# Kernel tuning notes

Hardware: AMD Instinct MI355X
Metric: run time of the kernel (lower is better)

Reference implementation:

```python
import jax, jax.numpy as jnp
import numpy as np

D_MODEL = 1024
HEAD_DIM = D_MODEL // 16  # num_heads=16, used only for the softmax scale
EPS = 1e-5


def _layernorm(x, g, b):
    mu = jnp.mean(x, axis=-1, keepdims=True)
    var = jnp.var(x, axis=-1, keepdims=True)
    return (x - mu) * jax.lax.rsqrt(var + EPS) * g + b


def setup_inputs() -> dict:
    key = jax.random.key(0)
    ks = jax.random.split(key, 16)
    d, dff = D_MODEL, 4 * D_MODEL
    s = 1.0 / np.sqrt(d)
    inp = {
        "x": jax.random.normal(ks[0], (4, 2048, d), dtype=jnp.float32),
        "wq": jax.random.normal(ks[1], (d, d), dtype=jnp.float32) * s,
        "bq": jnp.zeros((d,), jnp.float32),
        "wk": jax.random.normal(ks[2], (d, d), dtype=jnp.float32) * s,
        "bk": jnp.zeros((d,), jnp.float32),
        "wv": jax.random.normal(ks[3], (d, d), dtype=jnp.float32) * s,
        "bv": jnp.zeros((d,), jnp.float32),
        "wo": jax.random.normal(ks[4], (d, d), dtype=jnp.float32) * s,
        "bo": jnp.zeros((d,), jnp.float32),
        "w1": jax.random.normal(ks[5], (d, dff), dtype=jnp.float32) * s,
        "b1": jnp.zeros((dff,), jnp.float32),
        "w2": jax.random.normal(ks[6], (dff, d), dtype=jnp.float32) * (1.0 / np.sqrt(dff)),
        "b2": jnp.zeros((d,), jnp.float32),
        "g1": jnp.ones((d,), jnp.float32),
        "be1": jnp.zeros((d,), jnp.float32),
        "g2": jnp.ones((d,), jnp.float32),
        "be2": jnp.zeros((d,), jnp.float32),
    }
    return inp


def reference(x, wq, bq, wk, bk, wv, bv, wo, bo, w1, b1, w2, b2, g1, be1, g2, be2):
    # --- attention sub-block (NOTE: no head split in original module) ---
    residual = x
    h = _layernorm(x, g1, be1)
    q = h @ wq + bq
    k = h @ wk + bk
    v = h @ wv + bv
    scale = 1.0 / np.sqrt(HEAD_DIM)
    scores = jnp.einsum("bsd,btd->bst", q, k) * scale  # [B,S,S]
    attn = jax.nn.softmax(scores, axis=-1)
    ctx = jnp.einsum("bst,btd->bsd", attn, v)
    x = ctx @ wo + bo + residual
    # --- MLP sub-block ---
    residual = x
    h = _layernorm(x, g2, be2)
    h = jax.nn.gelu(h @ w1 + b1, approximate=False)
    return h @ w2 + b2 + residual
```

## Files before the change

kernel.cpp:

```cpp
#include <hip/hip_runtime.h>
#include <hip/hip_bf16.h>

typedef __hip_bfloat16 bf16;
typedef __attribute__((ext_vector_type(8))) short short8;
typedef __attribute__((ext_vector_type(4))) float floatx4;
typedef __attribute__((address_space(3))) char c3;

template <int V> struct ic { static constexpr int value = V; };

__device__ __forceinline__ unsigned short f2bf(float x) {
  unsigned u = __builtin_bit_cast(unsigned, x);
  unsigned r = (u + 0x7fffu + ((u >> 16) & 1u)) >> 16;
  return (unsigned short)r;
}

#define GLL(g, l) __builtin_amdgcn_global_load_lds(                                  \
    (const __attribute__((address_space(1))) void*)(g),                              \
    (__attribute__((address_space(3))) void*)(l), 16, 0, 0)

template <int N> __device__ __forceinline__ void vmwait() {
  asm volatile("s_waitcnt vmcnt(%0)" ::"i"(N) : "memory");
}
template <int N> __device__ __forceinline__ void lgkwait() {
  asm volatile("s_waitcnt lgkmcnt(%0)" ::"i"(N) : "memory");
  __builtin_amdgcn_sched_barrier(0);
}
template <int OFF> __device__ __forceinline__ short8 dsr(unsigned a) {
  short8 r;
  asm volatile("ds_read_b128 %0, %1 offset:%2" : "=v"(r) : "v"(a), "i"(OFF));
  return r;
}
#define MFMA_(d, a, b) d = __builtin_amdgcn_mfma_f32_16x16x32_bf16(a, b, d, 0, 0, 0)

__global__ __launch_bounds__(256) void wtrans_kernel(const float* __restrict__ in,
                                                     bf16* __restrict__ out,
                                                     int K, int N) {
  __shared__ float tile[32][33];
  int tx = threadIdx.x, ty = threadIdx.y;
  int n0 = blockIdx.x * 32, k0 = blockIdx.y * 32;
#pragma unroll
  for (int i = 0; i < 32; i += 8)
    tile[ty + i][tx] = in[(size_t)(k0 + ty + i) * N + (n0 + tx)];
  __syncthreads();
#pragma unroll
  for (int i = 0; i < 32; i += 8)
    out[(size_t)(n0 + ty + i) * K + (k0 + tx)] = __float2bfloat16(tile[tx][ty + i]);
}

__global__ __launch_bounds__(256) void ln_kernel(const float* __restrict__ x,
                                                 const float* __restrict__ g,
                                                 const float* __restrict__ b,
                                                 bf16* __restrict__ out) {
  const int D = 1024;
  size_t row = blockIdx.x;
  int t = threadIdx.x;
  float4 v = ((const float4*)(x + row * D))[t];
  float s  = v.x + v.y + v.z + v.w;
  float ss = v.x * v.x + v.y * v.y + v.z * v.z + v.w * v.w;
#pragma unroll
  for (int off = 32; off > 0; off >>= 1) {
    s  += __shfl_xor(s, off);
    ss += __shfl_xor(ss, off);
  }
  __shared__ float rs[4], rss[4];
  int wv = t >> 6;
  if ((t & 63) == 0) { rs[wv] = s; rss[wv] = ss; }
  __syncthreads();
  s  = rs[0] + rs[1] + rs[2] + rs[3];
  ss = rss[0] + rss[1] + rss[2] + rss[3];
  float mu  = s * (1.f / D);
  float inv = rsqrtf(ss * (1.f / D) - mu * mu + 1e-5f);
  float4 gv = ((const float4*)g)[t];
  float4 bv = ((const float4*)b)[t];
  ushort4 o;
  o.x = f2bf((v.x - mu) * inv * gv.x + bv.x);
  o.y = f2bf((v.y - mu) * inv * gv.y + bv.y);
  o.z = f2bf((v.z - mu) * inv * gv.z + bv.z);
  o.w = f2bf((v.w - mu) * inv * gv.w + bv.w);
  ((ushort4*)(out + row * D))[t] = o;
}

__global__ __launch_bounds__(256) void softmax_kernel(float* sc) {
  const int S = 2048;
  float* p = sc + (size_t)blockIdx.x * S;
  int t = threadIdx.x;
  float4 v0 = ((const float4*)p)[2 * t];
  float4 v1 = ((const float4*)p)[2 * t + 1];
  float f[8] = {v0.x, v0.y, v0.z, v0.w, v1.x, v1.y, v1.z, v1.w};
  float m = f[0];
#pragma unroll
  for (int j = 1; j < 8; ++j) m = fmaxf(m, f[j]);
#pragma unroll
  for (int off = 32; off > 0; off >>= 1) m = fmaxf(m, __shfl_xor(m, off));
  __shared__ float r1[4], r2[4];
  int wv = t >> 6;
  if ((t & 63) == 0) r1[wv] = m;
  __syncthreads();
  m = fmaxf(fmaxf(r1[0], r1[1]), fmaxf(r1[2], r1[3]));
  float s = 0.f;
#pragma unroll
  for (int j = 0; j < 8; ++j) { f[j] = __expf(f[j] - m); s += f[j]; }
#pragma unroll
  for (int off = 32; off > 0; off >>= 1) s += __shfl_xor(s, off);
  if ((t & 63) == 0) r2[wv] = s;
  __syncthreads();
  s = r2[0] + r2[1] + r2[2] + r2[3];
  float inv = 1.f / s;
  unsigned u0 = f2bf(f[0] * inv), u1 = f2bf(f[1] * inv);
  unsigned u2 = f2bf(f[2] * inv), u3 = f2bf(f[3] * inv);
  unsigned u4 = f2bf(f[4] * inv), u5 = f2bf(f[5] * inv);
  unsigned u6 = f2bf(f[6] * inv), u7 = f2bf(f[7] * inv);
  uint4 o;
  o.x = u0 | (u1 << 16);
  o.y = u2 | (u3 << 16);
  o.z = u4 | (u5 << 16);
  o.w = u6 | (u7 << 16);
  ((uint4*)p)[t] = o;
}

template <bool OUT_BF16, bool HAS_BIAS, bool HAS_RES, bool GELU, bool VTR>
__global__ __launch_bounds__(512, 2) void gemm9w(
    const bf16* __restrict__ A, int lda, size_t sA,
    const bf16* __restrict__ BT, int ldb, size_t sB,
    void* Cv, size_t sC,
    const float* __restrict__ bias, const float* res, bf16* vtr,
    int N, int K, float alpha, int gx, int gy) {
  __shared__ __align__(16) char ldsb[131072];
  const unsigned lds0 = (unsigned)(uintptr_t)(c3*)ldsb;

  const int tid = threadIdx.x;
  const int lane = tid & 63;
  const int wave = tid >> 6;
  const int wm = wave >> 2, wn = wave & 3;
  const int lr = lane & 15, lq = lane >> 4;

  int id = blockIdx.x;
  const int nwg = gridDim.x;
  if ((nwg & 7) == 0) id = (id & 7) * (nwg >> 3) + (id >> 3);
  const int bx = id % gx;
  const int rem = id / gx;
  const int by = rem % gy;
  const int bz = rem / gy;
  const int m0 = by * 256, n0 = bx * 256;

  const int sidx = tid >> 3;
  const int schunk = ((tid & 7) ^ (sidx & 7)) * 8;
  const bf16* gA = A + sA * bz + (size_t)(m0 + sidx) * lda + schunk;
  const int rowB = ((sidx >> 5) << 6) + (sidx & 31);
  const bf16* gB = BT + sB * bz + (size_t)(n0 + rowB) * ldb + schunk;

  const int nk = K >> 6;

  auto stA = [&](int tt, int h) {
    if (tt < nk) {
      const bf16* s = gA + (size_t)(h * 64) * lda + (size_t)tt * 64;
      char* d = ldsb + (((tt & 1) * 2 + h) << 14) + tid * 16;
      GLL(s, d);
      GLL(s + (size_t)128 * lda, d + 8192);
    }
  };
  auto stB = [&](int tt, int g) {
    if (tt < nk) {
      const bf16* s = gB + (size_t)(g * 32) * ldb + (size_t)tt * 64;
      char* d = ldsb + 65536 + (((tt & 1) * 2 + g) << 14) + tid * 16;
      GLL(s, d);
      GLL(s + (size_t)128 * ldb, d + 8192);
    }
  };

  const unsigned aoff = (wm * 64 + lr) * 128 + ((lq ^ (lr & 7)) << 4);
  const unsigned boff = (wn * 32 + lr) * 128 + ((lq ^ (lr & 7)) << 4);

  floatx4 acc[2][2][4][2] = {};

  stA(0, 0); stB(0, 0); stB(0, 1); stA(0, 1);
  stA(1, 0); stB(1, 0); stB(1, 1);
  vmwait<6>();
  __builtin_amdgcn_s_barrier();

  auto body = [&](int kt, auto modeC) {
    constexpr int MODE = decltype(modeC)::value;
    const unsigned p = (unsigned)(kt & 1);
    const unsigned Aa = lds0 + ((p * 2 + 0) << 14);
    const unsigned Ab = lds0 + ((p * 2 + 1) << 14);
    const unsigned Bg = lds0 + 65536 + ((p * 2 + 0) << 14);
    const unsigned Bd = lds0 + 65536 + ((p * 2 + 1) << 14);
    short8 a0[4], a1[4], g0[2], g1[2], d0[2], d1[2];

    {
      const unsigned aA = Aa + aoff, aX = aA ^ 64;
      a0[0] = dsr<0>(aA); a0[1] = dsr<2048>(aA); a0[2] = dsr<4096>(aA); a0[3] = dsr<6144>(aA);
      a1[0] = dsr<0>(aX); a1[1] = dsr<2048>(aX); a1[2] = dsr<4096>(aX); a1[3] = dsr<6144>(aX);
      const unsigned bA = Bg + boff, bX = bA ^ 64;
      g0[0] = dsr<0>(bA); g0[1] = dsr<2048>(bA);
      g1[0] = dsr<0>(bX); g1[1] = dsr<2048>(bX);
    }
    stA(kt + 1, 1);
    __builtin_amdgcn_s_barrier();
    lgkwait<0>();
    __builtin_amdgcn_s_setprio(1);
#pragma unroll
    for (int mi = 0; mi < 4; ++mi)
#pragma unroll
      for (int nl = 0; nl < 2; ++nl) MFMA_(acc[0][0][mi][nl], a0[mi], g0[nl]);
#pragma unroll
    for (int mi = 0; mi < 4; ++mi)
#pragma unroll
      for (int nl = 0; nl < 2; ++nl) MFMA_(acc[0][0][mi][nl], a1[mi], g1[nl]);
    __builtin_amdgcn_s_setprio(0);
    __builtin_amdgcn_s_barrier();

    {
      const unsigned bA = Bd + boff, bX = bA ^ 64;
      d0[0] = dsr<0>(bA); d0[1] = dsr<2048>(bA);
      d1[0] = dsr<0>(bX); d1[1] = dsr<2048>(bX);
    }
    stA(kt + 2, 0);
    __builtin_amdgcn_s_barrier();
    lgkwait<0>();
    __builtin_amdgcn_s_setprio(1);
#pragma unroll
    for (int mi = 0; mi < 4; ++mi)
#pragma unroll
      for (int nl = 0; nl < 2; ++nl) MFMA_(acc[0][1][mi][nl], a0[mi], d0[nl]);
#pragma unroll
    for (int mi = 0; mi < 4; ++mi)
#pragma unroll
      for (int nl = 0; nl < 2; ++nl) MFMA_(acc[0][1][mi][nl], a1[mi], d1[nl]);
    __builtin_amdgcn_s_setprio(0);
    __builtin_amdgcn_s_barrier();

    {
      const unsigned aA = Ab + aoff, aX = aA ^ 64;
      a0[0] = dsr<0>(aA); a0[1] = dsr<2048>(aA); a0[2] = dsr<4096>(aA); a0[3] = dsr<6144>(aA);
      a1[0] = dsr<0>(aX); a1[1] = dsr<2048>(aX); a1[2] = dsr<4096>(aX); a1[3] = dsr<6144>(aX);
    }
    stB(kt + 2, 0);
    __builtin_amdgcn_s_barrier();
    lgkwait<0>();
    __builtin_amdgcn_s_setprio(1);
#pragma unroll
    for (int mi = 0; mi < 4; ++mi)
#pragma unroll
      for (int nl = 0; nl < 2; ++nl) MFMA_(acc[1][1][mi][nl], a0[mi], d0[nl]);
#pragma unroll
    for (int mi = 0; mi < 4; ++mi)
#pragma unroll
      for (int nl = 0; nl < 2; ++nl) MFMA_(acc[1][1][mi][nl], a1[mi], d1[nl]);
    __builtin_amdgcn_s_setprio(0);
    __builtin_amdgcn_s_barrier();

    stB(kt + 2, 1);
    __builtin_amdgcn_s_barrier();
    __builtin_amdgcn_s_setprio(1);
#pragma unroll
    for (int mi = 0; mi < 4; ++mi)
#pragma unroll
      for (int nl = 0; nl < 2; ++nl) MFMA_(acc[1][0][mi][nl], a0[mi], g0[nl]);
#pragma unroll
    for (int mi = 0; mi < 4; ++mi)
#pragma unroll
      for (int nl = 0; nl < 2; ++nl) MFMA_(acc[1][0][mi][nl], a1[mi], g1[nl]);
    __builtin_amdgcn_s_setprio(0);
    if constexpr (MODE == 0) vmwait<6>();
    else if constexpr (MODE == 1) vmwait<0>();
    __builtin_amdgcn_s_barrier();
  };

  for (int kt = 0; kt + 2 < nk; ++kt) body(kt, ic<0>{});
  body(nk - 2, ic<1>{});
  body(nk - 1, ic<2>{});

  float* Cf = (float*)Cv;
  bf16* Cb = (bf16*)Cv;
  const size_t cb = sC * bz;
#pragma unroll
  for (int mh = 0; mh < 2; ++mh)
#pragma unroll
    for (int ng = 0; ng < 2; ++ng)
#pragma unroll
      for (int mi = 0; mi < 4; ++mi) {
        const int row = m0 + wm * 128 + (mh * 4 + mi) * 16 + lq * 4;
#pragma unroll
        for (int nl = 0; nl < 2; ++nl) {
          const int col = n0 + wn * 64 + (ng * 2 + nl) * 16 + lr;
          const float bb = HAS_BIAS ? bias[col] : 0.f;
#pragma unroll
          for (int r = 0; r < 4; ++r) {
            float val = acc[mh][ng][mi][nl][r] * alpha + bb;
            if (GELU) val = 0.5f * val * (1.f + erff(val * 0.70710678118654752f));
            if (HAS_RES) val += res[(size_t)(row + r) * N + col];
            const size_t idx = cb + (size_t)(row + r) * N + col;
            if (OUT_BF16) Cb[idx] = __float2bfloat16(val);
            else Cf[idx] = val;
            if (VTR) {
              if (col >= 2048) {
                const int rr = row + r;
                vtr[(((size_t)(rr >> 11) << 10) + (col - 2048)) * 2048 + (rr & 2047)] =
                    __float2bfloat16(val);
              }
            }
          }
        }
      }
}

template <bool OUT_BF16, bool HAS_BIAS, bool HAS_RES, bool GELU, bool VTR>
__global__ __launch_bounds__(512, 2) void gemm9n(
    const bf16* __restrict__ A, int lda, size_t sA,
    const bf16* __restrict__ BT, int ldb, size_t sB,
    void* Cv, size_t sC,
    const float* __restrict__ bias, const float* res, bf16* vtr,
    int N, int K, float alpha, int gx, int gy) {
  __shared__ __align__(16) char ldsb[98304];
  const unsigned lds0 = (unsigned)(uintptr_t)(c3*)ldsb;

  const int tid = threadIdx.x;
  const int lane = tid & 63;
  const int wave = tid >> 6;
  const int wm = wave >> 2, wn = wave & 3;
  const int lr = lane & 15, lq = lane >> 4;

  int id = blockIdx.x;
  const int nwg = gridDim.x;
  if ((nwg & 7) == 0) id = (id & 7) * (nwg >> 3) + (id >> 3);
  const int bx = id % gx;
  const int rem = id / gx;
  const int by = rem % gy;
  const int bz = rem / gy;
  const int m0 = by * 256, n0 = bx * 128;

  const int sidx = tid >> 3;
  const int schunk = ((tid & 7) ^ (sidx & 7)) * 8;
  const bf16* gA = A + sA * bz + (size_t)(m0 + sidx) * lda + schunk;
  const bf16* gB = BT + sB * bz + (size_t)(n0 + sidx) * ldb + schunk;

  const int nk = K >> 6;

  auto stA = [&](int tt, int h) {
    if (tt < nk) {
      const bf16* s = gA + (size_t)(h * 64) * lda + (size_t)tt * 64;
      char* d = ldsb + (((tt & 1) * 2 + h) << 14) + tid * 16;
      GLL(s, d);
      GLL(s + (size_t)128 * lda, d + 8192);
    }
  };
  auto stBn = [&](int tt) {
    if (tt < nk) {
      const bf16* s = gB + (size_t)tt * 64;
      char* d = ldsb + 65536 + ((tt & 1) << 14) + tid * 16;
      GLL(s, d);
      GLL(s + (size_t)64 * ldb, d + 8192);
    }
  };

  const unsigned aoff = (wm * 64 + lr) * 128 + ((lq ^ (lr & 7)) << 4);
  const unsigned boff = (wn * 32 + lr) * 128 + ((lq ^ (lr & 7)) << 4);

  floatx4 acc[2][4][2] = {};

  stA(0, 0); stBn(0); stA(0, 1);
  stA(1, 0); stBn(1);
  vmwait<4>();
  __builtin_amdgcn_s_barrier();

  auto body = [&](int kt, auto modeC) {
    constexpr int MODE = decltype(modeC)::value;
    const unsigned p = (unsigned)(kt & 1);
    const unsigned Aa = lds0 + ((p * 2 + 0) << 14);
    const unsigned Ab = lds0 + ((p * 2 + 1) << 14);
    const unsigned Bb = lds0 + 65536 + (p << 14);
    short8 a0[4], a1[4], b0[2], b1[2];

    {
      const unsigned aA = Aa + aoff, aX = aA ^ 64;
      a0[0] = dsr<0>(aA); a0[1] = dsr<2048>(aA); a0[2] = dsr<4096>(aA); a0[3] = dsr<6144>(aA);
      a1[0] = dsr<0>(aX); a1[1] = dsr<2048>(aX); a1[2] = dsr<4096>(aX); a1[3] = dsr<6144>(aX);
      const unsigned bA = Bb + boff, bX = bA ^ 64;
      b0[0] = dsr<0>(bA); b0[1] = dsr<2048>(bA);
      b1[0] = dsr<0>(bX); b1[1] = dsr<2048>(bX);
    }
    stA(kt + 1, 1);
    __builtin_amdgcn_s_barrier();
    lgkwait<0>();
    __builtin_amdgcn_s_setprio(1);
#pragma unroll
    for (int mi = 0; mi < 4; ++mi)
#pragma unroll
      for (int nl = 0; nl < 2; ++nl) MFMA_(acc[0][mi][nl], a0[mi], b0[nl]);
#pragma unroll
    for (int mi = 0; mi < 4; ++mi)
#pragma unroll
      for (int nl = 0; nl < 2; ++nl) MFMA_(acc[0][mi][nl], a1[mi], b1[nl]);
    __builtin_amdgcn_s_setprio(0);
    __builtin_amdgcn_s_barrier();

    {
      const unsigned aA = Ab + aoff, aX = aA ^ 64;
      a0[0] = dsr<0>(aA); a0[1] = dsr<2048>(aA); a0[2] = dsr<4096>(aA); a0[3] = dsr<6144>(aA);
      a1[0] = dsr<0>(aX); a1[1] = dsr<2048>(aX); a1[2] = dsr<4096>(aX); a1[3] = dsr<6144>(aX);
    }
    stA(kt + 2, 0); stBn(kt + 2);
    __builtin_amdgcn_s_barrier();
    lgkwait<0>();
    __builtin_amdgcn_s_setprio(1);
#pragma unroll
    for (int mi = 0; mi < 4; ++mi)
#pragma unroll
      for (int nl = 0; nl < 2; ++nl) MFMA_(acc[1][mi][nl], a0[mi], b0[nl]);
#pragma unroll
    for (int mi = 0; mi < 4; ++mi)
#pragma unroll
      for (int nl = 0; nl < 2; ++nl) MFMA_(acc[1][mi][nl], a1[mi], b1[nl]);
    __builtin_amdgcn_s_setprio(0);
    if constexpr (MODE == 0) vmwait<4>();
    else if constexpr (MODE == 1) vmwait<0>();
    __builtin_amdgcn_s_barrier();
  };

  for (int kt = 0; kt + 2 < nk; ++kt) body(kt, ic<0>{});
  body(nk - 2, ic<1>{});
  body(nk - 1, ic<2>{});

  float* Cf = (float*)Cv;
  bf16* Cb = (bf16*)Cv;
  const size_t cb = sC * bz;
#pragma unroll
  for (int mh = 0; mh < 2; ++mh)
#pragma unroll
    for (int mi = 0; mi < 4; ++mi) {
      const int row = m0 + wm * 128 + (mh * 4 + mi) * 16 + lq * 4;
#pragma unroll
      for (int nl = 0; nl < 2; ++nl) {
        const int col = n0 + wn * 32 + nl * 16 + lr;
        const float bb = HAS_BIAS ? bias[col] : 0.f;
#pragma unroll
        for (int r = 0; r < 4; ++r) {
          float val = acc[mh][mi][nl][r] * alpha + bb;
          if (GELU) val = 0.5f * val * (1.f + erff(val * 0.70710678118654752f));
          if (HAS_RES) val += res[(size_t)(row + r) * N + col];
          const size_t idx = cb + (size_t)(row + r) * N + col;
          if (OUT_BF16) Cb[idx] = __float2bfloat16(val);
          else Cf[idx] = val;
          if (VTR) {
            if (col >= 2048) {
              const int rr = row + r;
              vtr[(((size_t)(rr >> 11) << 10) + (col - 2048)) * 2048 + (rr & 2047)] =
                  __float2bfloat16(val);
            }
          }
        }
      }
    }
}

extern "C" void kernel_launch(void* const* d_in, const int* in_sizes, int n_in,
                              void* d_out, int out_size, void* d_ws, size_t ws_size,
                              hipStream_t stream) {
  const int B = 4, S = 2048, D = 1024, DFF = 4096;
  const int M = B * S;
  const float* x   = (const float*)d_in[0];
  const float* wq  = (const float*)d_in[1];
  const float* bq  = (const float*)d_in[2];
  const float* wk  = (const float*)d_in[3];
  const float* bk  = (const float*)d_in[4];
  const float* wv  = (const float*)d_in[5];
  const float* bv  = (const float*)d_in[6];
  const float* wo  = (const float*)d_in[7];
  const float* bo  = (const float*)d_in[8];
  const float* w1  = (const float*)d_in[9];
  const float* b1  = (const float*)d_in[10];
  const float* w2  = (const float*)d_in[11];
  const float* b2  = (const float*)d_in[12];
  const float* g1  = (const float*)d_in[13];
  const float* be1 = (const float*)d_in[14];
  const float* g2  = (const float*)d_in[15];
  const float* be2 = (const float*)d_in[16];
  float* out = (float*)d_out;

  char* wsb = (char*)d_ws;
  const size_t MB1 = 1ull << 20;
  bf16* wqkvT = (bf16*)(wsb + 0 * MB1);
  bf16* woT   = (bf16*)(wsb + 6 * MB1);
  bf16* w1T   = (bf16*)(wsb + 8 * MB1);
  bf16* w2T   = (bf16*)(wsb + 16 * MB1);
  float* bqkv = (float*)(wsb + 24 * MB1);
  bf16* h     = (bf16*)(wsb + 25 * MB1);
  bf16* qkv   = (bf16*)(wsb + 41 * MB1);
  bf16* hidden = (bf16*)(wsb + 41 * MB1);
  bf16* vTall = (bf16*)(wsb + 89 * MB1);
  float* sc   = (float*)(wsb + 105 * MB1);

  int chunk = 1;
  if (ws_size > 105 * MB1) {
    size_t c = (ws_size - 105 * MB1) / (16 * MB1);
    chunk = (int)(c > 4 ? 4 : (c < 1 ? 1 : c));
  }

  dim3 tb(32, 8);
  wtrans_kernel<<<dim3(32, 32), tb, 0, stream>>>(wq, wqkvT, D, D);
  wtrans_kernel<<<dim3(32, 32), tb, 0, stream>>>(wk, wqkvT + (size_t)1024 * 1024, D, D);
  wtrans_kernel<<<dim3(32, 32), tb, 0, stream>>>(wv, wqkvT + (size_t)2048 * 1024, D, D);
  wtrans_kernel<<<dim3(32, 32), tb, 0, stream>>>(wo, woT, D, D);
  wtrans_kernel<<<dim3(128, 32), tb, 0, stream>>>(w1, w1T, D, DFF);
  wtrans_kernel<<<dim3(32, 128), tb, 0, stream>>>(w2, w2T, DFF, D);
  hipMemcpyAsync(bqkv, bq, 4096, hipMemcpyDeviceToDevice, stream);
  hipMemcpyAsync(bqkv + 1024, bk, 4096, hipMemcpyDeviceToDevice, stream);
  hipMemcpyAsync(bqkv + 2048, bv, 4096, hipMemcpyDeviceToDevice, stream);

  ln_kernel<<<M, 256, 0, stream>>>(x, g1, be1, h);

  gemm9w<true, true, false, false, true><<<12 * 32, 512, 0, stream>>>(
      h, D, 0, wqkvT, D, 0, qkv, 0, bqkv, nullptr, vTall, 3072, D, 1.f, 12, 32);

  for (int b0 = 0; b0 < B; b0 += chunk) {
    int c = (B - b0 < chunk) ? (B - b0) : chunk;
    gemm9w<false, false, false, false, false><<<64 * c, 512, 0, stream>>>(
        qkv + (size_t)b0 * S * 3072, 3072, (size_t)S * 3072,
        qkv + (size_t)b0 * S * 3072 + 1024, 3072, (size_t)S * 3072,
        sc, (size_t)S * S, nullptr, nullptr, nullptr, S, D, 0.125f, 8, 8);
    softmax_kernel<<<c * S, 256, 0, stream>>>(sc);
    gemm9n<true, false, false, false, false><<<64 * c, 512, 0, stream>>>(
        (const bf16*)sc, 2 * S, (size_t)S * 2 * S,
        vTall + (size_t)b0 * D * S, S, (size_t)D * S,
        h + (size_t)b0 * S * D, (size_t)S * D, nullptr, nullptr, nullptr, D, S, 1.f, 8, 8);
  }

  gemm9n<false, true, true, false, false><<<8 * 32, 512, 0, stream>>>(
      h, D, 0, woT, D, 0, out, 0, bo, x, nullptr, D, D, 1.f, 8, 32);

  ln_kernel<<<M, 256, 0, stream>>>(out, g2, be2, h);

  gemm9w<true, true, false, true, false><<<16 * 32, 512, 0, stream>>>(
      h, D, 0, w1T, D, 0, hidden, 0, b1, nullptr, nullptr, DFF, D, 1.f, 16, 32);

  gemm9n<false, true, true, false, false><<<8 * 32, 512, 0, stream>>>(
      hidden, DFF, 0, w2T, DFF, 0, out, 0, b2, out, nullptr, D, DFF, 1.f, 8, 32);
}
```

Before: 469.6 us.

## Switch GEMM kernels to 32x32x16 MFMA with K-split LDS staging

Both GEMM kernels move from 16x16x32 bf16 MFMA to 32x32x16 bf16 MFMA. The LDS tiles are restaged so that each K-tile is split into two 32-wide K halves with a 4-chunk XOR swizzle, and each body iteration now has two phases instead of four, with fewer barriers. The goal is fewer MFMA instructions and fewer LDS reads per FLOP, plus less synchronisation. The risks are LDS bank conflicts from the new swizzle and a changed wait-count pipeline, and the epilogue now writes strided 32x32 output fragments.

```diff
diff --git a/kernel.cpp b/kernel.cpp
--- a/kernel.cpp
+++ b/kernel.cpp
@@ -3,7 +3,7 @@
 
 typedef __hip_bfloat16 bf16;
 typedef __attribute__((ext_vector_type(8))) short short8;
-typedef __attribute__((ext_vector_type(4))) float floatx4;
+typedef __attribute__((ext_vector_type(16))) float floatx16;
 typedef __attribute__((address_space(3))) char c3;
 
 template <int V> struct ic { static constexpr int value = V; };
@@ -30,7 +30,7 @@
   asm volatile("ds_read_b128 %0, %1 offset:%2" : "=v"(r) : "v"(a), "i"(OFF));
   return r;
 }
-#define MFMA_(d, a, b) d = __builtin_amdgcn_mfma_f32_16x16x32_bf16(a, b, d, 0, 0, 0)
+#define MFMA32(d, a, b) d = __builtin_amdgcn_mfma_f32_32x32x16_bf16(a, b, d, 0, 0, 0)
 
 __global__ __launch_bounds__(256) void wtrans_kernel(const float* __restrict__ in,
                                                      bf16* __restrict__ out,
@@ -119,7 +119,7 @@
 }
 
 template <bool OUT_BF16, bool HAS_BIAS, bool HAS_RES, bool GELU, bool VTR>
-__global__ __launch_bounds__(512, 2) void gemm9w(
+__global__ __launch_bounds__(512, 2) void gemmA(
     const bf16* __restrict__ A, int lda, size_t sA,
     const bf16* __restrict__ BT, int ldb, size_t sB,
     void* Cv, size_t sC,
@@ -127,12 +127,13 @@
     int N, int K, float alpha, int gx, int gy) {
   __shared__ __align__(16) char ldsb[131072];
   const unsigned lds0 = (unsigned)(uintptr_t)(c3*)ldsb;
+  const unsigned ldsB0 = lds0 + 65536;
 
   const int tid = threadIdx.x;
   const int lane = tid & 63;
   const int wave = tid >> 6;
   const int wm = wave >> 2, wn = wave & 3;
-  const int lr = lane & 15, lq = lane >> 4;
+  const int l5 = lane >> 5, l31 = lane & 31;
 
   int id = blockIdx.x;
   const int nwg = gridDim.x;
@@ -143,128 +144,96 @@
   const int bz = rem / gy;
   const int m0 = by * 256, n0 = bx * 256;
 
-  const int sidx = tid >> 3;
-  const int schunk = ((tid & 7) ^ (sidx & 7)) * 8;
-  const bf16* gA = A + sA * bz + (size_t)(m0 + sidx) * lda + schunk;
-  const int rowB = ((sidx >> 5) << 6) + (sidx & 31);
-  const bf16* gB = BT + sB * bz + (size_t)(n0 + rowB) * ldb + schunk;
-
+  const int sr = tid >> 2;
+  const int scc = ((tid & 3) ^ (sr & 3)) * 8;
+  const bf16* gA = A + sA * bz + (size_t)(m0 + sr) * lda + scc;
+  const bf16* gB = BT + sB * bz + (size_t)(n0 + sr) * ldb + scc;
   const int nk = K >> 6;
 
-  auto stA = [&](int tt, int h) {
+  auto stA = [&](int tt, int kh) {
     if (tt < nk) {
-      const bf16* s = gA + (size_t)(h * 64) * lda + (size_t)tt * 64;
-      char* d = ldsb + (((tt & 1) * 2 + h) << 14) + tid * 16;
+      const bf16* s = gA + (size_t)tt * 64 + kh * 32;
+      char* d = ldsb + (((tt & 1) * 2 + kh) << 14) + tid * 16;
       GLL(s, d);
       GLL(s + (size_t)128 * lda, d + 8192);
     }
   };
-  auto stB = [&](int tt, int g) {
+  auto stB = [&](int tt, int kh) {
     if (tt < nk) {
-      const bf16* s = gB + (size_t)(g * 32) * ldb + (size_t)tt * 64;
-      char* d = ldsb + 65536 + (((tt & 1) * 2 + g) << 14) + tid * 16;
+      const bf16* s = gB + (size_t)tt * 64 + kh * 32;
+      char* d = ldsb + 65536 + (((tt & 1) * 2 + kh) << 14) + tid * 16;
       GLL(s, d);
       GLL(s + (size_t)128 * ldb, d + 8192);
     }
   };
 
-  const unsigned aoff = (wm * 64 + lr) * 128 + ((lq ^ (lr & 7)) << 4);
-  const unsigned boff = (wn * 32 + lr) * 128 + ((lq ^ (lr & 7)) << 4);
-
-  floatx4 acc[2][2][4][2] = {};
-
-  stA(0, 0); stB(0, 0); stB(0, 1); stA(0, 1);
-  stA(1, 0); stB(1, 0); stB(1, 1);
-  vmwait<6>();
+  const unsigned uswz = (unsigned)((l5 ^ (lane & 3)) << 4);
+  const unsigned aRow = (unsigned)((wm * 128 + l31) * 64) + uswz;
+  const unsigned bRow = (unsigned)((wn * 64 + l31) * 64) + uswz;
+
+  floatx16 acc[4][2] = {};
+
+  stA(0, 0); stB(0, 0);
+  stA(0, 1); stB(0, 1);
+  stA(1, 0); stB(1, 0);
+  vmwait<8>();
   __builtin_amdgcn_s_barrier();
 
   auto body = [&](int kt, auto modeC) {
     constexpr int MODE = decltype(modeC)::value;
     const unsigned p = (unsigned)(kt & 1);
-    const unsigned Aa = lds0 + ((p * 2 + 0) << 14);
-    const unsigned Ab = lds0 + ((p * 2 + 1) << 14);
-    const unsigned Bg = lds0 + 65536 + ((p * 2 + 0) << 14);
-    const unsigned Bd = lds0 + 65536 + ((p * 2 + 1) << 14);
-    short8 a0[4], a1[4], g0[2], g1[2], d0[2], d1[2];
+    const unsigned Ak0 = lds0 + ((p * 2 + 0) << 14);
+    const unsigned Ak1 = lds0 + ((p * 2 + 1) << 14);
+    const unsigned Bk0 = ldsB0 + ((p * 2 + 0) << 14);
+    const unsigned Bk1 = ldsB0 + ((p * 2 + 1) << 14);
+    short8 a0[4], a1[4], b0[2], b1[2];
 
     {
-      const unsigned aA = Aa + aoff, aX = aA ^ 64;
+      const unsigned aA = Ak0 + aRow, aX = aA ^ 32;
       a0[0] = dsr<0>(aA); a0[1] = dsr<2048>(aA); a0[2] = dsr<4096>(aA); a0[3] = dsr<6144>(aA);
       a1[0] = dsr<0>(aX); a1[1] = dsr<2048>(aX); a1[2] = dsr<4096>(aX); a1[3] = dsr<6144>(aX);
-      const unsigned bA = Bg + boff, bX = bA ^ 64;
-      g0[0] = dsr<0>(bA); g0[1] = dsr<2048>(bA);
-      g1[0] = dsr<0>(bX); g1[1] = dsr<2048>(bX);
-    }
-    stA(kt + 1, 1);
-    __builtin_amdgcn_s_barrier();
+      const unsigned bA = Bk0 + bRow, bX = bA ^ 32;
+      b0[0] = dsr<0>(bA); b0[1] = dsr<2048>(bA);
+      b1[0] = dsr<0>(bX); b1[1] = dsr<2048>(bX);
+    }
+    stA(kt + 1, 1); stB(kt + 1, 1);
     lgkwait<0>();
     __builtin_amdgcn_s_setprio(1);
 #pragma unroll
-    for (int mi = 0; mi < 4; ++mi)
-#pragma unroll
-      for (int nl = 0; nl < 2; ++nl) MFMA_(acc[0][0][mi][nl], a0[mi], g0[nl]);
-#pragma unroll
-    for (int mi = 0; mi < 4; ++mi)
-#pragma unroll
-      for (int nl = 0; nl < 2; ++nl) MFMA_(acc[0][0][mi][nl], a1[mi], g1[nl]);
+    for (int mf = 0; mf < 4; ++mf)
+#pragma unroll
+      for (int nf = 0; nf < 2; ++nf) MFMA32(acc[mf][nf], a0[mf], b0[nf]);
+#pragma unroll
+    for (int mf = 0; mf < 4; ++mf)
+#pragma unroll
+      for (int nf = 0; nf < 2; ++nf) MFMA32(acc[mf][nf], a1[mf], b1[nf]);
     __builtin_amdgcn_s_setprio(0);
+    if constexpr (MODE < 2) vmwait<8>();
+    else vmwait<0>();
     __builtin_amdgcn_s_barrier();
 
     {
-      const unsigned bA = Bd + boff, bX = bA ^ 64;
-      d0[0] = dsr<0>(bA); d0[1] = dsr<2048>(bA);
-      d1[0] = dsr<0>(bX); d1[1] = dsr<2048>(bX);
-    }
-    stA(kt + 2, 0);
-    __builtin_amdgcn_s_barrier();
+      const unsigned aA = Ak1 + aRow, aX = aA ^ 32;
+      a0[0] = dsr<0>(aA); a0[1] = dsr<2048>(aA); a0[2] = dsr<4096>(aA); a0[3] = dsr<6144>(aA);
+      a1[0] = dsr<0>(aX); a1[1] = dsr<2048>(aX); a1[2] = dsr<4096>(aX); a1[3] = dsr<6144>(aX);
+      const unsigned bA = Bk1 + bRow, bX = bA ^ 32;
+      b0[0] = dsr<0>(bA); b0[1] = dsr<2048>(bA);
+      b1[0] = dsr<0>(bX); b1[1] = dsr<2048>(bX);
+    }
+    stA(kt + 2, 0); stB(kt + 2, 0);
     lgkwait<0>();
     __builtin_amdgcn_s_setprio(1);
 #pragma unroll
-    for (int mi = 0; mi < 4; ++mi)
-#pragma unroll
-      for (int nl = 0; nl < 2; ++nl) MFMA_(acc[0][1][mi][nl], a0[mi], d0[nl]);
-#pragma unroll
-    for (int mi = 0; mi < 4; ++mi)
-#pragma unroll
-      for (int nl = 0; nl < 2; ++nl) MFMA_(acc[0][1][mi][nl], a1[mi], d1[nl]);
+    for (int mf = 0; mf < 4; ++mf)
+#pragma unroll
+      for (int nf = 0; nf < 2; ++nf) MFMA32(acc[mf][nf], a0[mf], b0[nf]);
+#pragma unroll
+    for (int mf = 0; mf < 4; ++mf)
+#pragma unroll
+      for (int nf = 0; nf < 2; ++nf) MFMA32(acc[mf][nf], a1[mf], b1[nf]);
     __builtin_amdgcn_s_setprio(0);
-    __builtin_amdgcn_s_barrier();
-
-    {
-      const unsigned aA = Ab + aoff, aX = aA ^ 64;
-      a0[0] = dsr<0>(aA); a0[1] = dsr<2048>(aA); a0[2] = dsr<4096>(aA); a0[3] = dsr<6144>(aA);
-      a1[0] = dsr<0>(aX); a1[1] = dsr<2048>(aX); a1[2] = dsr<4096>(aX); a1[3] = dsr<6144>(aX);
-    }
-    stB(kt + 2, 0);
-    __builtin_amdgcn_s_barrier();
-    lgkwait<0>();
-    __builtin_amdgcn_s_setprio(1);
-#pragma unroll
-    for (int mi = 0; mi < 4; ++mi)
-#pragma unroll
-      for (int nl = 0; nl < 2; ++nl) MFMA_(acc[1][1][mi][nl], a0[mi], d0[nl]);
-#pragma unroll
-    for (int mi = 0; mi < 4; ++mi)
-#pragma unroll
-      for (int nl = 0; nl < 2; ++nl) MFMA_(acc[1][1][mi][nl], a1[mi], d1[nl]);
-    __builtin_amdgcn_s_setprio(0);
-    __builtin_amdgcn_s_barrier();
-
-    stB(kt + 2, 1);
-    __builtin_amdgcn_s_barrier();
-    __builtin_amdgcn_s_setprio(1);
-#pragma unroll
-    for (int mi = 0; mi < 4; ++mi)
-#pragma unroll
-      for (int nl = 0; nl < 2; ++nl) MFMA_(acc[1][0][mi][nl], a0[mi], g0[nl]);
-#pragma unroll
-    for (int mi = 0; mi < 4; ++mi)
-#pragma unroll
-      for (int nl = 0; nl < 2; ++nl) MFMA_(acc[1][0][mi][nl], a1[mi], g1[nl]);
-    __builtin_amdgcn_s_setprio(0);
-    if constexpr (MODE == 0) vmwait<6>();
-    else if constexpr (MODE == 1) vmwait<0>();
-    __builtin_amdgcn_s_barrier();
+    if constexpr (MODE == 0) { vmwait<8>(); __builtin_amdgcn_s_barrier(); }
+    else if constexpr (MODE == 1) { vmwait<4>(); __builtin_amdgcn_s_barrier(); }
   };
 
   for (int kt = 0; kt + 2 < nk; ++kt) body(kt, ic<0>{});
@@ -274,52 +243,49 @@
   float* Cf = (float*)Cv;
   bf16* Cb = (bf16*)Cv;
   const size_t cb = sC * bz;
-#pragma unroll
-  for (int mh = 0; mh < 2; ++mh)
-#pragma unroll
-    for (int ng = 0; ng < 2; ++ng)
-#pragma unroll
-      for (int mi = 0; mi < 4; ++mi) {
-        const int row = m0 + wm * 128 + (mh * 4 + mi) * 16 + lq * 4;
-#pragma unroll
-        for (int nl = 0; nl < 2; ++nl) {
-          const int col = n0 + wn * 64 + (ng * 2 + nl) * 16 + lr;
-          const float bb = HAS_BIAS ? bias[col] : 0.f;
-#pragma unroll
-          for (int r = 0; r < 4; ++r) {
-            float val = acc[mh][ng][mi][nl][r] * alpha + bb;
-            if (GELU) val = 0.5f * val * (1.f + erff(val * 0.70710678118654752f));
-            if (HAS_RES) val += res[(size_t)(row + r) * N + col];
-            const size_t idx = cb + (size_t)(row + r) * N + col;
-            if (OUT_BF16) Cb[idx] = __float2bfloat16(val);
-            else Cf[idx] = val;
-            if (VTR) {
-              if (col >= 2048) {
-                const int rr = row + r;
-                vtr[(((size_t)(rr >> 11) << 10) + (col - 2048)) * 2048 + (rr & 2047)] =
-                    __float2bfloat16(val);
-              }
-            }
+  const int colb = n0 + wn * 64 + l31;
+  const int rowb = m0 + wm * 128 + (l5 << 2);
+#pragma unroll
+  for (int mf = 0; mf < 4; ++mf)
+#pragma unroll
+    for (int nf = 0; nf < 2; ++nf) {
+      const int col = colb + nf * 32;
+      const float bb = HAS_BIAS ? bias[col] : 0.f;
+#pragma unroll
+      for (int r = 0; r < 16; ++r) {
+        const int row = rowb + mf * 32 + (r & 3) + ((r >> 2) << 3);
+        float val = acc[mf][nf][r] * alpha + bb;
+        if (GELU) val = 0.5f * val * (1.f + erff(val * 0.70710678118654752f));
+        if (HAS_RES) val += res[(size_t)row * N + col];
+        const size_t idx = cb + (size_t)row * N + col;
+        if (OUT_BF16) Cb[idx] = __float2bfloat16(val);
+        else Cf[idx] = val;
+        if (VTR) {
+          if (col >= 2048) {
+            vtr[(((size_t)(row >> 11) << 10) + (col - 2048)) * 2048 + (row & 2047)] =
+                __float2bfloat16(val);
           }
         }
       }
-}
-
-template <bool OUT_BF16, bool HAS_BIAS, bool HAS_RES, bool GELU, bool VTR>
-__global__ __launch_bounds__(512, 2) void gemm9n(
+    }
+}
+
+template <bool OUT_BF16, bool HAS_BIAS, bool HAS_RES, bool GELU>
+__global__ __launch_bounds__(512, 2) void gemmB(
     const bf16* __restrict__ A, int lda, size_t sA,
     const bf16* __restrict__ BT, int ldb, size_t sB,
     void* Cv, size_t sC,
-    const float* __restrict__ bias, const float* res, bf16* vtr,
+    const float* __restrict__ bias, const float* res,
     int N, int K, float alpha, int gx, int gy) {
   __shared__ __align__(16) char ldsb[98304];
   const unsigned lds0 = (unsigned)(uintptr_t)(c3*)ldsb;
+  const unsigned ldsB0 = lds0 + 65536;
 
   const int tid = threadIdx.x;
   const int lane = tid & 63;
   const int wave = tid >> 6;
   const int wm = wave >> 2, wn = wave & 3;
-  const int lr = lane & 15, lq = lane >> 4;
+  const int l5 = lane >> 5, l31 = lane & 31;
 
   int id = blockIdx.x;
   const int nwg = gridDim.x;
@@ -330,92 +296,85 @@
   const int bz = rem / gy;
   const int m0 = by * 256, n0 = bx * 128;
 
-  const int sidx = tid >> 3;
-  const int schunk = ((tid & 7) ^ (sidx & 7)) * 8;
-  const bf16* gA = A + sA * bz + (size_t)(m0 + sidx) * lda + schunk;
-  const bf16* gB = BT + sB * bz + (size_t)(n0 + sidx) * ldb + schunk;
-
+  const int sr = tid >> 2;
+  const int scc = ((tid & 3) ^ (sr & 3)) * 8;
+  const bf16* gA = A + sA * bz + (size_t)(m0 + sr) * lda + scc;
+  const bf16* gB = BT + sB * bz + (size_t)(n0 + sr) * ldb + scc;
   const int nk = K >> 6;
 
-  auto stA = [&](int tt, int h) {
+  auto stA = [&](int tt, int kh) {
     if (tt < nk) {
-      const bf16* s = gA + (size_t)(h * 64) * lda + (size_t)tt * 64;
-      char* d = ldsb + (((tt & 1) * 2 + h) << 14) + tid * 16;
+      const bf16* s = gA + (size_t)tt * 64 + kh * 32;
+      char* d = ldsb + (((tt & 1) * 2 + kh) << 14) + tid * 16;
       GLL(s, d);
       GLL(s + (size_t)128 * lda, d + 8192);
     }
   };
-  auto stBn = [&](int tt) {
+  auto stB = [&](int tt, int kh) {
     if (tt < nk) {
-      const bf16* s = gB + (size_t)tt * 64;
-      char* d = ldsb + 65536 + ((tt & 1) << 14) + tid * 16;
+      const bf16* s = gB + (size_t)tt * 64 + kh * 32;
+      char* d = ldsb + 65536 + (((tt & 1) * 2 + kh) << 13) + tid * 16;
       GLL(s, d);
-      GLL(s + (size_t)64 * ldb, d + 8192);
-    }
-  };
-
-  const unsigned aoff = (wm * 64 + lr) * 128 + ((lq ^ (lr & 7)) << 4);
-  const unsigned boff = (wn * 32 + lr) * 128 + ((lq ^ (lr & 7)) << 4);
-
-  floatx4 acc[2][4][2] = {};
-
-  stA(0, 0); stBn(0); stA(0, 1);
-  stA(1, 0); stBn(1);
-  vmwait<4>();
+    }
+  };
+
+  const unsigned uswz = (unsigned)((l5 ^ (lane & 3)) << 4);
+  const unsigned aRow = (unsigned)((wm * 128 + l31) * 64) + uswz;
+  const unsigned bRow = (unsigned)((wn * 32 + l31) * 64) + uswz;
+
+  floatx16 acc[4] = {};
+
+  stA(0, 0); stB(0, 0);
+  stA(0, 1); stB(0, 1);
+  stA(1, 0); stB(1, 0);
+  vmwait<6>();
   __builtin_amdgcn_s_barrier();
 
   auto body = [&](int kt, auto modeC) {
     constexpr int MODE = decltype(modeC)::value;
     const unsigned p = (unsigned)(kt & 1);
-    const unsigned Aa = lds0 + ((p * 2 + 0) << 14);
-    const unsigned Ab = lds0 + ((p * 2 + 1) << 14);
-    const unsigned Bb = lds0 + 65536 + (p << 14);
-    short8 a0[4], a1[4], b0[2], b1[2];
+    const unsigned Ak0 = lds0 + ((p * 2 + 0) << 14);
+    const unsigned Ak1 = lds0 + ((p * 2 + 1) << 14);
+    const unsigned Bk0 = ldsB0 + ((p * 2 + 0) << 13);
+    const unsigned Bk1 = ldsB0 + ((p * 2 + 1) << 13);
+    short8 a0[4], a1[4], b0, b1;
 
     {
-      const unsigned aA = Aa + aoff, aX = aA ^ 64;
+      const unsigned aA = Ak0 + aRow, aX = aA ^ 32;
       a0[0] = dsr<0>(aA); a0[1] = dsr<2048>(aA); a0[2] = dsr<4096>(aA); a0[3] = dsr<6144>(aA);
       a1[0] = dsr<0>(aX); a1[1] = dsr<2048>(aX); a1[2] = dsr<4096>(aX); a1[3] = dsr<6144>(aX);
-      const unsigned bA = Bb + boff, bX = bA ^ 64;
-      b0[0] = dsr<0>(bA); b0[1] = dsr<2048>(bA);
-      b1[0] = dsr<0>(bX); b1[1] = dsr<2048>(bX);
-    }
-    stA(kt + 1, 1);
-    __builtin_amdgcn_s_barrier();
+      const unsigned bA = Bk0 + bRow;
+      b0 = dsr<0>(bA); b1 = dsr<0>(bA ^ 32);
+    }
+    stA(kt + 1, 1); stB(kt + 1, 1);
     lgkwait<0>();
     __builtin_amdgcn_s_setprio(1);
 #pragma unroll
-    for (int mi = 0; mi < 4; ++mi)
-#pragma unroll
-      for (int nl = 0; nl < 2; ++nl) MFMA_(acc[0][mi][nl], a0[mi], b0[nl]);
-#pragma unroll
-    for (int mi = 0; mi < 4; ++mi)
-#pragma unroll
-      for (int nl = 0; nl < 2; ++nl) MFMA_(acc[0][mi][nl], a1[mi], b1[nl]);
+    for (int mf = 0; mf < 4; ++mf) MFMA32(acc[mf], a0[mf], b0);
+#pragma unroll
+    for (int mf = 0; mf < 4; ++mf) MFMA32(acc[mf], a1[mf], b1);
     __builtin_amdgcn_s_setprio(0);
+    if constexpr (MODE < 2) vmwait<6>();
+    else vmwait<0>();
     __builtin_amdgcn_s_barrier();
 
     {
-      const unsigned aA = Ab + aoff, aX = aA ^ 64;
+      const unsigned aA = Ak1 + aRow, aX = aA ^ 32;
       a0[0] = dsr<0>(aA); a0[1] = dsr<2048>(aA); a0[2] = dsr<4096>(aA); a0[3] = dsr<6144>(aA);
       a1[0] = dsr<0>(aX); a1[1] = dsr<2048>(aX); a1[2] = dsr<4096>(aX); a1[3] = dsr<6144>(aX);
-    }
-    stA(kt + 2, 0); stBn(kt + 2);
-    __builtin_amdgcn_s_barrier();
+      const unsigned bA = Bk1 + bRow;
+      b0 = dsr<0>(bA); b1 = dsr<0>(bA ^ 32);
+    }
+    stA(kt + 2, 0); stB(kt + 2, 0);
     lgkwait<0>();
     __builtin_amdgcn_s_setprio(1);
 #pragma unroll
-    for (int mi = 0; mi < 4; ++mi)
-#pragma unroll
-      for (int nl = 0; nl < 2; ++nl) MFMA_(acc[1][mi][nl], a0[mi], b0[nl]);
-#pragma unroll
-    for (int mi = 0; mi < 4; ++mi)
-#pragma unroll
-      for (int nl = 0; nl < 2; ++nl) MFMA_(acc[1][mi][nl], a1[mi], b1[nl]);
+    for (int mf = 0; mf < 4; ++mf) MFMA32(acc[mf], a0[mf], b0);
+#pragma unroll
+    for (int mf = 0; mf < 4; ++mf) MFMA32(acc[mf], a1[mf], b1);
     __builtin_amdgcn_s_setprio(0);
-    if constexpr (MODE == 0) vmwait<4>();
-    else if constexpr (MODE == 1) vmwait<0>();
-    __builtin_amdgcn_s_barrier();
+    if constexpr (MODE == 0) { vmwait<6>(); __builtin_amdgcn_s_barrier(); }
+    else if constexpr (MODE == 1) { vmwait<3>(); __builtin_amdgcn_s_barrier(); }
   };
 
   for (int kt = 0; kt + 2 < nk; ++kt) body(kt, ic<0>{});
@@ -425,32 +384,20 @@
   float* Cf = (float*)Cv;
   bf16* Cb = (bf16*)Cv;
   const size_t cb = sC * bz;
-#pragma unroll
-  for (int mh = 0; mh < 2; ++mh)
-#pragma unroll
-    for (int mi = 0; mi < 4; ++mi) {
-      const int row = m0 + wm * 128 + (mh * 4 + mi) * 16 + lq * 4;
-#pragma unroll
-      for (int nl = 0; nl < 2; ++nl) {
-        const int col = n0 + wn * 32 + nl * 16 + lr;
-        const float bb = HAS_BIAS ? bias[col] : 0.f;
-#pragma unroll
-        for (int r = 0; r < 4; ++r) {
-          float val = acc[mh][mi][nl][r] * alpha + bb;
-          if (GELU) val = 0.5f * val * (1.f + erff(val * 0.70710678118654752f));
-          if (HAS_RES) val += res[(size_t)(row + r) * N + col];
-          const size_t idx = cb + (size_t)(row + r) * N + col;
-          if (OUT_BF16) Cb[idx] = __float2bfloat16(val);
-          else Cf[idx] = val;
-          if (VTR) {
-            if (col >= 2048) {
-              const int rr = row + r;
-              vtr[(((size_t)(rr >> 11) << 10) + (col - 2048)) * 2048 + (rr & 2047)] =
-                  __float2bfloat16(val);
-            }
-          }
-        }
-      }
+  const int col = n0 + wn * 32 + l31;
+  const int rowb = m0 + wm * 128 + (l5 << 2);
+  const float bb = HAS_BIAS ? bias[col] : 0.f;
+#pragma unroll
+  for (int mf = 0; mf < 4; ++mf)
+#pragma unroll
+    for (int r = 0; r < 16; ++r) {
+      const int row = rowb + mf * 32 + (r & 3) + ((r >> 2) << 3);
+      float val = acc[mf][r] * alpha + bb;
+      if (GELU) val = 0.5f * val * (1.f + erff(val * 0.70710678118654752f));
+      if (HAS_RES) val += res[(size_t)row * N + col];
+      const size_t idx = cb + (size_t)row * N + col;
+      if (OUT_BF16) Cb[idx] = __float2bfloat16(val);
+      else Cf[idx] = val;
     }
 }
 
@@ -510,30 +457,30 @@
 
   ln_kernel<<<M, 256, 0, stream>>>(x, g1, be1, h);
 
-  gemm9w<true, true, false, false, true><<<12 * 32, 512, 0, stream>>>(
+  gemmA<true, true, false, false, true><<<12 * 32, 512, 0, stream>>>(
       h, D, 0, wqkvT, D, 0, qkv, 0, bqkv, nullptr, vTall, 3072, D, 1.f, 12, 32);
 
   for (int b0 = 0; b0 < B; b0 += chunk) {
     int c = (B - b0 < chunk) ? (B - b0) : chunk;
-    gemm9w<false, false, false, false, false><<<64 * c, 512, 0, stream>>>(
+    gemmA<false, false, false, false, false><<<64 * c, 512, 0, stream>>>(
         qkv + (size_t)b0 * S * 3072, 3072, (size_t)S * 3072,
         qkv + (size_t)b0 * S * 3072 + 1024, 3072, (size_t)S * 3072,
         sc, (size_t)S * S, nullptr, nullptr, nullptr, S, D, 0.125f, 8, 8);
     softmax_kernel<<<c * S, 256, 0, stream>>>(sc);
-    gemm9n<true, false, false, false, false><<<64 * c, 512, 0, stream>>>(
+    gemmB<true, false, false, false><<<64 * c, 512, 0, stream>>>(
         (const bf16*)sc, 2 * S, (size_t)S * 2 * S,
         vTall + (size_t)b0 * D * S, S, (size_t)D * S,
-        h + (size_t)b0 * S * D, (size_t)S * D, nullptr, nullptr, nullptr, D, S, 1.f, 8, 8);
+        h + (size_t)b0 * S * D, (size_t)S * D, nullptr, nullptr, D, S, 1.f, 8, 8);
   }
 
-  gemm9n<false, true, true, false, false><<<8 * 32, 512, 0, stream>>>(
-      h, D, 0, woT, D, 0, out, 0, bo, x, nullptr, D, D, 1.f, 8, 32);
+  gemmB<false, true, true, false><<<8 * 32, 512, 0, stream>>>(
+      h, D, 0, woT, D, 0, out, 0, bo, x, D, D, 1.f, 8, 32);
 
   ln_kernel<<<M, 256, 0, stream>>>(out, g2, be2, h);
 
-  gemm9w<true, true, false, true, false><<<16 * 32, 512, 0, stream>>>(
+  gemmA<true, true, false, true, false><<<16 * 32, 512, 0, stream>>>(
       h, D, 0, w1T, D, 0, hidden, 0, b1, nullptr, nullptr, DFF, D, 1.f, 16, 32);
 
-  gemm9n<false, true, true, false, false><<<8 * 32, 512, 0, stream>>>(
-      hidden, DFF, 0, w2T, DFF, 0, out, 0, b2, out, nullptr, D, DFF, 1.f, 8, 32);
-}
+  gemmB<false, true, true, false><<<8 * 32, 512, 0, stream>>>(
+      hidden, DFF, 0, w2T, DFF, 0, out, 0, b2, out, D, DFF, 1.f, 8, 32);
+}
```

Measured after the change: 556.6 us. +18.5%, slower.
